# Kernel optimization log

Hardware: AMD Instinct MI355X
Metric: run time of the kernel (lower is better)

## Reference

```python
import jax, jax.numpy as jnp
import numpy as np

H = 64  # hidden_size
E = 100  # ebd_size
MAX_LEN = 100


def setup_inputs() -> dict:
    key = jax.random.key(0)
    ks = jax.random.split(key, 7)
    B, L = 4096, 100
    return {
        "x": jax.random.normal(ks[0], (B, L, E), jnp.float32),
        "W_in": jax.random.normal(ks[1], (E, 3 * H), jnp.float32) * 0.1,
        "b_in": jax.random.normal(ks[2], (3 * H,), jnp.float32) * 0.1,
        "W_h": jax.random.normal(ks[3], (H, 3 * H), jnp.float32) * 0.1,
        "b_h": jax.random.normal(ks[4], (3 * H,), jnp.float32) * 0.1,
        "W_fc": jax.random.normal(ks[5], (H, 2), jnp.float32) * 0.1,
        "b_fc": jax.random.normal(ks[6], (2,), jnp.float32) * 0.1,
    }


def _standardize(t):
    # torch: (t - t.mean(1, keepdim)) / t.std(1, keepdim)  (std is unbiased, ddof=1)
    m = jnp.mean(t, axis=1, keepdims=True)
    s = jnp.std(t, axis=1, keepdims=True, ddof=1)
    return (t - m) / s


def _gru_step(h, xt, W_in, b_in, W_h, b_h, norm):
    ti = xt @ W_in + b_in            # [B, 3H]
    th = h @ W_h + b_h               # [B, 3H]
    if norm:
        ti = _standardize(ti)
        th = _standardize(th)
    r_i, z_i, n_i = jnp.split(ti, 3, axis=1)
    r_h, z_h, n_h = jnp.split(th, 3, axis=1)
    r_t = jax.nn.sigmoid(r_i + r_h)
    z_t = jax.nn.sigmoid(z_i + z_h)
    n_t = jnp.tanh(n_i + r_t * n_h)
    return (1.0 - z_t) * n_t + z_t * h


def reference(x, W_in, b_in, W_h, b_h, W_fc, b_fc):
    B, L, _ = x.shape
    L_eff = min(L, MAX_LEN + 1)  # loop breaks when l > max_length
    xs = jnp.transpose(x[:, :L_eff, :], (1, 0, 2))  # [L, B, E]
    h0 = jnp.zeros((B, H), x.dtype)

    # loop 1: no norm
    h1, _ = jax.lax.scan(
        lambda h, xt: (_gru_step(h, xt, W_in, b_in, W_h, b_h, norm=False), None),
        h0, xs)
    # loop 2: vector norm; note original code does NOT reset hid_i
    h2, _ = jax.lax.scan(
        lambda h, xt: (_gru_step(h, xt, W_in, b_in, W_h, b_h, norm=True), None),
        h1, xs)
    return h2 @ W_fc + b_fc
```

## Files before the change

kernel.cpp:

```cpp
#include <hip/hip_runtime.h>

#define L_SEQ 100
#define E_DIM 100
#define G_DIM 192
#define B_TOT 4096

typedef __attribute__((ext_vector_type(8))) short bf16x8;
typedef __attribute__((ext_vector_type(4))) float f32x4;
typedef __attribute__((ext_vector_type(4))) float float4v;
typedef __attribute__((ext_vector_type(2))) float float2v;
typedef __attribute__((ext_vector_type(4))) unsigned uint4v;
typedef __attribute__((ext_vector_type(2))) unsigned uint2v;

#define MFMA16 __builtin_amdgcn_mfma_f32_16x16x32_bf16

static __device__ __forceinline__ unsigned short f2bf(float f) {
    union { float f; unsigned u; } v; v.f = f;
    unsigned r = v.u + 0x7FFFu + ((v.u >> 16) & 1u);
    return (unsigned short)(r >> 16);
}
static __device__ __forceinline__ unsigned cvtpk(float lo, float hi) {
    unsigned r;
    asm("v_cvt_pk_bf16_f32 %0, %1, %2" : "=v"(r) : "v"(lo), "v"(hi));
    return r;
}
static __device__ __forceinline__ bf16x8 as_bf16x8(uint4v u) {
    union { uint4v u; bf16x8 h; } v; v.u = u; return v.h;
}
static __device__ __forceinline__ float rcpf_(float x) { return __builtin_amdgcn_rcpf(x); }

#define BAR() do { \
    asm volatile("s_waitcnt lgkmcnt(0)" ::: "memory"); \
    __builtin_amdgcn_s_barrier(); \
    asm volatile("" ::: "memory"); \
} while (0)

struct XBuf { f32x4 v[6]; f32x4 tail; };

static __device__ __forceinline__ int tmod(int c) {
    int t = c;
    if (t >= L_SEQ) t -= L_SEQ;
    if (t >= L_SEQ) t -= L_SEQ;
    return t;
}

static __device__ __forceinline__ void x_pf(
    XBuf& b, const float* __restrict__ xlane, const float* __restrict__ xrow, int c, bool g0)
{
    const int t = tmod(c);
    const float* p = xlane + t * E_DIM;
    b.v[0] = *(const f32x4*)(p);
    b.v[1] = *(const f32x4*)(p + 4);
    b.v[2] = *(const f32x4*)(p + 32);
    b.v[3] = *(const f32x4*)(p + 36);
    b.v[4] = *(const f32x4*)(p + 64);
    b.v[5] = *(const f32x4*)(p + 68);
    const f32x4 z = {0.f, 0.f, 0.f, 0.f};
    b.tail = g0 ? *(const f32x4*)(xrow + t * E_DIM + 96) : z;
}

static __device__ __forceinline__ void produce(
    XBuf& xb, const float* __restrict__ xlane, const float* __restrict__ xrow,
    int c, bool g0, float* __restrict__ tird, float* __restrict__ sltiw,
    const bf16x8 (&awin)[3][4], const float (&binq)[12])
{
    bf16x8 bx0 = as_bf16x8((uint4v){cvtpk(xb.v[0][0], xb.v[0][1]), cvtpk(xb.v[0][2], xb.v[0][3]),
                                    cvtpk(xb.v[1][0], xb.v[1][1]), cvtpk(xb.v[1][2], xb.v[1][3])});
    bf16x8 bx1 = as_bf16x8((uint4v){cvtpk(xb.v[2][0], xb.v[2][1]), cvtpk(xb.v[2][2], xb.v[2][3]),
                                    cvtpk(xb.v[3][0], xb.v[3][1]), cvtpk(xb.v[3][2], xb.v[3][3])});
    bf16x8 bx2 = as_bf16x8((uint4v){cvtpk(xb.v[4][0], xb.v[4][1]), cvtpk(xb.v[4][2], xb.v[4][3]),
                                    cvtpk(xb.v[5][0], xb.v[5][1]), cvtpk(xb.v[5][2], xb.v[5][3])});
    bf16x8 bx3 = as_bf16x8((uint4v){cvtpk(xb.tail[0], xb.tail[1]), cvtpk(xb.tail[2], xb.tail[3]),
                                    0u, 0u});
    x_pf(xb, xlane, xrow, c + 2, g0);

    const f32x4 zero = {0.f, 0.f, 0.f, 0.f};
    f32x4 t0 = MFMA16(awin[0][0], bx0, zero, 0, 0, 0);
    f32x4 t1 = MFMA16(awin[1][0], bx0, zero, 0, 0, 0);
    f32x4 t2 = MFMA16(awin[2][0], bx0, zero, 0, 0, 0);
    t0 = MFMA16(awin[0][1], bx1, t0, 0, 0, 0);
    t1 = MFMA16(awin[1][1], bx1, t1, 0, 0, 0);
    t2 = MFMA16(awin[2][1], bx1, t2, 0, 0, 0);
    t0 = MFMA16(awin[0][2], bx2, t0, 0, 0, 0);
    t1 = MFMA16(awin[1][2], bx2, t1, 0, 0, 0);
    t2 = MFMA16(awin[2][2], bx2, t2, 0, 0, 0);
    t0 = MFMA16(awin[0][3], bx3, t0, 0, 0, 0);
    t1 = MFMA16(awin[1][3], bx3, t1, 0, 0, 0);
    t2 = MFMA16(awin[2][3], bx3, t2, 0, 0, 0);

    const int par = c & 1;
    float4v A0 = {t0[0] + binq[0], t0[1] + binq[1], t0[2] + binq[2],  t0[3] + binq[3]};
    float4v A1 = {t1[0] + binq[4], t1[1] + binq[5], t1[2] + binq[6],  t1[3] + binq[7]};
    float4v A2 = {t2[0] + binq[8], t2[1] + binq[9], t2[2] + binq[10], t2[3] + binq[11]};
    float* dst = tird + par * 3328;
    *(float4v*)(dst)     = A0;
    *(float4v*)(dst + 4) = A1;
    *(float4v*)(dst + 8) = A2;

    float s = ((A0[0] + A0[1]) + (A0[2] + A0[3])) + ((A1[0] + A1[1]) + (A1[2] + A1[3]))
            + ((A2[0] + A2[1]) + (A2[2] + A2[3]));
    float ss = 0.f;
    #pragma unroll
    for (int k2 = 0; k2 < 4; ++k2) ss = fmaf(A0[k2], A0[k2], ss);
    #pragma unroll
    for (int k2 = 0; k2 < 4; ++k2) ss = fmaf(A1[k2], A1[k2], ss);
    #pragma unroll
    for (int k2 = 0; k2 < 4; ++k2) ss = fmaf(A2[k2], A2[k2], ss);
    s  += __shfl_xor(s, 16);  s  += __shfl_xor(s, 32);
    ss += __shfl_xor(ss, 16); ss += __shfl_xor(ss, 32);
    if (g0) *(float2v*)(sltiw + par * 192) = (float2v){s, ss};
}

__global__ __launch_bounds__(512, 1) void gru_ws(
    const float* __restrict__ x,
    const float* __restrict__ Win, const float* __restrict__ bin,
    const float* __restrict__ Wh,  const float* __restrict__ bh,
    const float* __restrict__ Wfc, const float* __restrict__ bfc,
    float* __restrict__ out)
{
    __shared__ __align__(16) unsigned short hs[2][16][72];
    __shared__ __align__(16) float tir[2][4][16][52];
    __shared__ __align__(16) float slti[2][16][12];
    __shared__ __align__(16) float slth[2][16][12];

    const int tid = threadIdx.x;
    const int wv  = tid >> 6;
    const int w   = wv & 3;
    const bool tirole = (wv >= 4);
    const int l = tid & 63, c16 = l & 15, g = l >> 4;
    const bool g0 = (g == 0);
    const int row0 = blockIdx.x * 16;

    bf16x8 awin[3][4]; float binq[12];
    bf16x8 awh[3][2];  float bhq[12];
    const float* xrow = nullptr; const float* xlane = nullptr;

    if (tirole) {
        #pragma unroll
        for (int i = 0; i < 3; ++i)
          #pragma unroll
          for (int kt = 0; kt < 4; ++kt)
            #pragma unroll
            for (int j = 0; j < 8; ++j) {
                int k = 32 * kt + 8 * g + j;
                float v = (k < E_DIM) ? Win[k * G_DIM + 16 * (w + 4 * i) + c16] : 0.f;
                awin[i][kt][j] = (short)f2bf(v);
            }
        #pragma unroll
        for (int i = 0; i < 3; ++i)
          #pragma unroll
          for (int rr = 0; rr < 4; ++rr)
              binq[4 * i + rr] = bin[16 * (w + 4 * i) + 4 * g + rr];
        xrow  = x + (size_t)(row0 + c16) * (L_SEQ * E_DIM);
        xlane = xrow + 8 * g;
    } else {
        #pragma unroll
        for (int i = 0; i < 3; ++i)
          #pragma unroll
          for (int kt = 0; kt < 2; ++kt)
            #pragma unroll
            for (int j = 0; j < 8; ++j)
                awh[i][kt][j] = (short)f2bf(Wh[(32 * kt + 8 * g + j) * G_DIM + 16 * (w + 4 * i) + c16]);
        #pragma unroll
        for (int i = 0; i < 3; ++i)
          #pragma unroll
          for (int rr = 0; rr < 4; ++rr)
              bhq[4 * i + rr] = bh[16 * (w + 4 * i) + 4 * g + rr];
        bf16x8 z = {0, 0, 0, 0, 0, 0, 0, 0};
        *(bf16x8*)&hs[0][c16][8 * g]      = z;
        *(bf16x8*)&hs[0][c16][32 + 8 * g] = z;
    }

    float* tird        = &tir[0][w][c16][g * 12];
    float* sltiw       = &slti[0][c16][2 * w];
    float* slthw       = &slth[0][c16][2 * w];
    const float* sltir = &slti[0][c16][0];
    const float* slthr = &slth[0][c16][0];

    float hreg[4] = {0.f, 0.f, 0.f, 0.f};

    XBuf xA, xB;
    if (tirole) {
        x_pf(xA, xlane, xrow, 0, g0);
        x_pf(xB, xlane, xrow, 1, g0);
        produce(xA, xlane, xrow, 0, g0, tird, sltiw, awin, binq);
    }
    BAR();
    if (!tirole) __builtin_amdgcn_s_setprio(1);

    auto HGEMM = [&](int par, float4v& a0, float4v& a1, float4v& a2, float (&b)[12]) {
        const float* src = tird + par * 3328;
        a0 = *(const float4v*)(src);
        a1 = *(const float4v*)(src + 4);
        a2 = *(const float4v*)(src + 8);
        bf16x8 h0 = *(const bf16x8*)&hs[par][c16][8 * g];
        bf16x8 h1 = *(const bf16x8*)&hs[par][c16][32 + 8 * g];
        const f32x4 zero = {0.f, 0.f, 0.f, 0.f};
        f32x4 t0 = MFMA16(awh[0][0], h0, zero, 0, 0, 0);
        f32x4 t1 = MFMA16(awh[1][0], h0, zero, 0, 0, 0);
        f32x4 t2 = MFMA16(awh[2][0], h0, zero, 0, 0, 0);
        t0 = MFMA16(awh[0][1], h1, t0, 0, 0, 0);
        t1 = MFMA16(awh[1][1], h1, t1, 0, 0, 0);
        t2 = MFMA16(awh[2][1], h1, t2, 0, 0, 0);
        #pragma unroll
        for (int rr = 0; rr < 4; ++rr) {
            b[rr]     = t0[rr] + bhq[rr];
            b[4 + rr] = t1[rr] + bhq[4 + rr];
            b[8 + rr] = t2[rr] + bhq[8 + rr];
        }
    };
    auto HWRITE = [&](int par, float (&hn)[4]) {
        *(uint2v*)&hs[par ^ 1][c16][16 * w + 4 * g] = (uint2v){cvtpk(hn[0], hn[1]), cvtpk(hn[2], hn[3])};
    };

    #pragma unroll 1
    for (int s = 0; s < L_SEQ; s += 2) {
        #pragma unroll
        for (int sub = 0; sub < 2; ++sub) {
            const int st = s + sub;
            XBuf& X = sub ? xA : xB;
            if (tirole) {
                produce(X, xlane, xrow, st + 1, g0, tird, sltiw, awin, binq);
            } else {
                const int par = st & 1;
                float4v a0, a1, a2; float b[12];
                HGEMM(par, a0, a1, a2, b);
                float hn[4];
                #pragma unroll
                for (int rr = 0; rr < 4; ++rr) {
                    float er = rcpf_(1.f + __expf(-(a0[rr] + b[rr])));
                    float zt = rcpf_(1.f + __expf(-(a1[rr] + b[4 + rr])));
                    float u  = fmaf(er, b[8 + rr], a2[rr]);
                    float tn = fmaf(2.f, rcpf_(1.f + __expf(-2.f * u)), -1.f);
                    hn[rr] = fmaf(zt, hreg[rr] - tn, tn);
                    hreg[rr] = hn[rr];
                }
                HWRITE(par, hn);
            }
            BAR();
        }
    }

    #pragma unroll 1
    for (int s = L_SEQ; s < 2 * L_SEQ; s += 2) {
        #pragma unroll
        for (int sub = 0; sub < 2; ++sub) {
            const int st = s + sub;
            XBuf& X = sub ? xA : xB;
            const int par = st & 1;
            float4v a0, a1, a2; float b[12];
            if (tirole) {
                produce(X, xlane, xrow, st + 1, g0, tird, sltiw, awin, binq);
            } else {
                HGEMM(par, a0, a1, a2, b);
                float sb = 0.f, ssb = 0.f;
                #pragma unroll
                for (int k2 = 0; k2 < 12; ++k2) { sb += b[k2]; ssb = fmaf(b[k2], b[k2], ssb); }
                sb  += __shfl_xor(sb, 16);  sb  += __shfl_xor(sb, 32);
                ssb += __shfl_xor(ssb, 16); ssb += __shfl_xor(ssb, 32);
                if (g0) *(float2v*)(slthw + par * 192) = (float2v){sb, ssb};
            }
            BAR();
            if (!tirole) {
                const float* sp = slthr + par * 192;
                float4v q0 = *(const float4v*)(sp);
                float4v q1 = *(const float4v*)(sp + 4);
                const float* ip = sltir + par * 192;
                float4v r0 = *(const float4v*)(ip);
                float4v r1 = *(const float4v*)(ip + 4);
                float Sth  = (q0[0] + q0[2]) + (q1[0] + q1[2]);
                float SSth = (q0[1] + q0[3]) + (q1[1] + q1[3]);
                float Sti  = (r0[0] + r0[2]) + (r1[0] + r1[2]);
                float SSti = (r0[1] + r0[3]) + (r1[1] + r1[3]);
                float mth = Sth * (1.f / G_DIM);
                float rth = __builtin_amdgcn_rsqf(
                    fmaxf((SSth - (float)G_DIM * mth * mth) * (1.f / (G_DIM - 1)), 1e-24f));
                float mti = Sti * (1.f / G_DIM);
                float rti = __builtin_amdgcn_rsqf(
                    fmaxf((SSti - (float)G_DIM * mti * mti) * (1.f / (G_DIM - 1)), 1e-24f));
                float mrti = mti * rti, mrth = mth * rth;
                float Cn = mrti + mrth;
                float hn[4];
                #pragma unroll
                for (int rr = 0; rr < 4; ++rr) {
                    float mr = fmaf(a0[rr], -rti, fmaf(b[rr],     -rth, Cn));
                    float er = rcpf_(1.f + __expf(mr));
                    float mz = fmaf(a1[rr], -rti, fmaf(b[4 + rr], -rth, Cn));
                    float zt = rcpf_(1.f + __expf(mz));
                    float ni = fmaf(a2[rr],     rti, -mrti);
                    float nh = fmaf(b[8 + rr],  rth, -mrth);
                    float u  = fmaf(er, nh, ni);
                    float tn = fmaf(2.f, rcpf_(1.f + __expf(-2.f * u)), -1.f);
                    hn[rr] = fmaf(zt, hreg[rr] - tn, tn);
                    hreg[rr] = hn[rr];
                }
                HWRITE(par, hn);
            }
            BAR();
        }
    }

    if (!tirole) {
        float po0 = 0.f, po1 = 0.f;
        #pragma unroll
        for (int rr = 0; rr < 4; ++rr) {
            int c = 16 * w + 4 * g + rr;
            po0 = fmaf(hreg[rr], Wfc[2 * c],     po0);
            po1 = fmaf(hreg[rr], Wfc[2 * c + 1], po1);
        }
        po0 += __shfl_xor(po0, 16); po0 += __shfl_xor(po0, 32);
        po1 += __shfl_xor(po1, 16); po1 += __shfl_xor(po1, 32);
        if (g0) *(float2v*)(slthw) = (float2v){po0, po1};
    }
    BAR();
    if (tid < 16) {
        const float* sp = &slth[0][tid][0];
        float4v q0 = *(const float4v*)(sp);
        float4v q1 = *(const float4v*)(sp + 4);
        out[(row0 + tid) * 2 + 0] = (q0[0] + q0[2]) + (q1[0] + q1[2]) + bfc[0];
        out[(row0 + tid) * 2 + 1] = (q0[1] + q0[3]) + (q1[1] + q1[3]) + bfc[1];
    }
}

extern "C" void kernel_launch(void* const* d_in, const int* in_sizes, int n_in,
                              void* d_out, int out_size, void* d_ws, size_t ws_size,
                              hipStream_t stream) {
    const float* x   = (const float*)d_in[0];
    const float* Win = (const float*)d_in[1];
    const float* bin = (const float*)d_in[2];
    const float* Wh  = (const float*)d_in[3];
    const float* bh  = (const float*)d_in[4];
    const float* Wfc = (const float*)d_in[5];
    const float* bfc = (const float*)d_in[6];
    float* out = (float*)d_out;
    gru_ws<<<dim3(B_TOT / 16), dim3(512), 0, stream>>>(
        x, Win, bin, Wh, bh, Wfc, bfc, out);
}
```

Measured before the change: 201.0 us.

## Prefetch input-gate projections one step ahead and fold log2e into weights

Producer warps now run two steps ahead instead of one. The recurrent warps load the next step's input-gate values and input-norm statistics right after writing h, instead of at the start of the next step. The input-side mean and rstd are precomputed inside that prefetch. All weights and biases are pre-scaled by log2(e) so the activations can use exp2 directly, which removes a multiply per exponent. This changes the slot/parity scheme and the barrier structure, and it risks extra register pressure plus bf16 rounding differences from the scaled weights.

New measurement: 238.3 us. +18.5%, slower.

```diff
diff --git a/kernel.cpp b/kernel.cpp
--- a/kernel.cpp
+++ b/kernel.cpp
@@ -4,6 +4,7 @@
 #define E_DIM 100
 #define G_DIM 192
 #define B_TOT 4096
+#define L2E   1.4426950408889634f
 
 typedef __attribute__((ext_vector_type(8))) short bf16x8;
 typedef __attribute__((ext_vector_type(4))) float f32x4;
@@ -36,9 +37,11 @@
 } while (0)
 
 struct XBuf { f32x4 v[6]; f32x4 tail; };
+struct TiRegs { float4v a0, a1, a2; float rtiF, cF; };
 
 static __device__ __forceinline__ int tmod(int c) {
     int t = c;
+    if (t >= L_SEQ) t -= L_SEQ;
     if (t >= L_SEQ) t -= L_SEQ;
     if (t >= L_SEQ) t -= L_SEQ;
     return t;
@@ -111,6 +114,25 @@
     if (g0) *(float2v*)(sltiw + par * 192) = (float2v){s, ss};
 }
 
+static __device__ __forceinline__ void lr_load(
+    TiRegs& R, int slot, const float* __restrict__ tird, const float* __restrict__ sltir)
+{
+    const float* src = tird + slot * 3328;
+    R.a0 = *(const float4v*)(src);
+    R.a1 = *(const float4v*)(src + 4);
+    R.a2 = *(const float4v*)(src + 8);
+    const float* sp = sltir + slot * 192;
+    float4v q0 = *(const float4v*)(sp);
+    float4v q1 = *(const float4v*)(sp + 4);
+    float S  = (q0[0] + q0[2]) + (q1[0] + q1[2]);
+    float SS = (q0[1] + q0[3]) + (q1[1] + q1[3]);
+    float m  = S * (1.f / G_DIM);
+    float var = (SS - (float)G_DIM * m * m) * (1.f / (G_DIM - 1));
+    float r = __builtin_amdgcn_rsqf(fmaxf(var, 1e-24f)) * L2E;
+    R.rtiF = r;
+    R.cF   = m * r;
+}
+
 __global__ __launch_bounds__(512, 1) void gru_ws(
     const float* __restrict__ x,
     const float* __restrict__ Win, const float* __restrict__ bin,
@@ -132,7 +154,7 @@
     const int row0 = blockIdx.x * 16;
 
     bf16x8 awin[3][4]; float binq[12];
-    bf16x8 awh[3][2];  float bhq[12];
+    bf16x8 awh[3][2];  float bhqL[12];
     const float* xrow = nullptr; const float* xlane = nullptr;
 
     if (tirole) {
@@ -143,14 +165,14 @@
             #pragma unroll
             for (int j = 0; j < 8; ++j) {
                 int k = 32 * kt + 8 * g + j;
-                float v = (k < E_DIM) ? Win[k * G_DIM + 16 * (w + 4 * i) + c16] : 0.f;
+                float v = (k < E_DIM) ? Win[k * G_DIM + 16 * (w + 4 * i) + c16] * L2E : 0.f;
                 awin[i][kt][j] = (short)f2bf(v);
             }
         #pragma unroll
         for (int i = 0; i < 3; ++i)
           #pragma unroll
           for (int rr = 0; rr < 4; ++rr)
-              binq[4 * i + rr] = bin[16 * (w + 4 * i) + 4 * g + rr];
+              binq[4 * i + rr] = bin[16 * (w + 4 * i) + 4 * g + rr] * L2E;
         xrow  = x + (size_t)(row0 + c16) * (L_SEQ * E_DIM);
         xlane = xrow + 8 * g;
     } else {
@@ -160,12 +182,12 @@
           for (int kt = 0; kt < 2; ++kt)
             #pragma unroll
             for (int j = 0; j < 8; ++j)
-                awh[i][kt][j] = (short)f2bf(Wh[(32 * kt + 8 * g + j) * G_DIM + 16 * (w + 4 * i) + c16]);
+                awh[i][kt][j] = (short)f2bf(Wh[(32 * kt + 8 * g + j) * G_DIM + 16 * (w + 4 * i) + c16] * L2E);
         #pragma unroll
         for (int i = 0; i < 3; ++i)
           #pragma unroll
           for (int rr = 0; rr < 4; ++rr)
-              bhq[4 * i + rr] = bh[16 * (w + 4 * i) + 4 * g + rr];
+              bhqL[4 * i + rr] = bh[16 * (w + 4 * i) + 4 * g + rr] * L2E;
         bf16x8 z = {0, 0, 0, 0, 0, 0, 0, 0};
         *(bf16x8*)&hs[0][c16][8 * g]      = z;
         *(bf16x8*)&hs[0][c16][32 + 8 * g] = z;
@@ -184,15 +206,17 @@
         x_pf(xA, xlane, xrow, 0, g0);
         x_pf(xB, xlane, xrow, 1, g0);
         produce(xA, xlane, xrow, 0, g0, tird, sltiw, awin, binq);
+        produce(xB, xlane, xrow, 1, g0, tird, sltiw, awin, binq);
     }
     BAR();
-    if (!tirole) __builtin_amdgcn_s_setprio(1);
-
-    auto HGEMM = [&](int par, float4v& a0, float4v& a1, float4v& a2, float (&b)[12]) {
-        const float* src = tird + par * 3328;
-        a0 = *(const float4v*)(src);
-        a1 = *(const float4v*)(src + 4);
-        a2 = *(const float4v*)(src + 8);
+
+    TiRegs RA, RB;
+    if (!tirole) {
+        lr_load(RA, 0, tird, sltir);
+        __builtin_amdgcn_s_setprio(1);
+    }
+
+    auto HGEMM = [&](int par, float (&b)[12]) {
         bf16x8 h0 = *(const bf16x8*)&hs[par][c16][8 * g];
         bf16x8 h1 = *(const bf16x8*)&hs[par][c16][32 + 8 * g];
         const f32x4 zero = {0.f, 0.f, 0.f, 0.f};
@@ -204,100 +228,91 @@
         t2 = MFMA16(awh[2][1], h1, t2, 0, 0, 0);
         #pragma unroll
         for (int rr = 0; rr < 4; ++rr) {
-            b[rr]     = t0[rr] + bhq[rr];
-            b[4 + rr] = t1[rr] + bhq[4 + rr];
-            b[8 + rr] = t2[rr] + bhq[8 + rr];
+            b[rr]     = t0[rr] + bhqL[rr];
+            b[4 + rr] = t1[rr] + bhqL[4 + rr];
+            b[8 + rr] = t2[rr] + bhqL[8 + rr];
         }
     };
     auto HWRITE = [&](int par, float (&hn)[4]) {
         *(uint2v*)&hs[par ^ 1][c16][16 * w + 4 * g] = (uint2v){cvtpk(hn[0], hn[1]), cvtpk(hn[2], hn[3])};
     };
 
+    auto H1 = [&](TiRegs& CUR, TiRegs& NXT, int st) {
+        const int par = st & 1;
+        float b[12];
+        HGEMM(par, b);
+        float hn[4];
+        #pragma unroll
+        for (int rr = 0; rr < 4; ++rr) {
+            float er = rcpf_(1.f + __builtin_exp2f(-(CUR.a0[rr] + b[rr])));
+            float zt = rcpf_(1.f + __builtin_exp2f(-(CUR.a1[rr] + b[4 + rr])));
+            float uL = fmaf(er, b[8 + rr], CUR.a2[rr]);
+            float tn = fmaf(2.f, rcpf_(1.f + __builtin_exp2f(-(uL + uL))), -1.f);
+            hn[rr] = fmaf(zt, hreg[rr] - tn, tn);
+            hreg[rr] = hn[rr];
+        }
+        HWRITE(par, hn);
+        lr_load(NXT, (st + 1) & 1, tird, sltir);
+    };
+
     #pragma unroll 1
     for (int s = 0; s < L_SEQ; s += 2) {
-        #pragma unroll
-        for (int sub = 0; sub < 2; ++sub) {
-            const int st = s + sub;
-            XBuf& X = sub ? xA : xB;
-            if (tirole) {
-                produce(X, xlane, xrow, st + 1, g0, tird, sltiw, awin, binq);
-            } else {
-                const int par = st & 1;
-                float4v a0, a1, a2; float b[12];
-                HGEMM(par, a0, a1, a2, b);
-                float hn[4];
-                #pragma unroll
-                for (int rr = 0; rr < 4; ++rr) {
-                    float er = rcpf_(1.f + __expf(-(a0[rr] + b[rr])));
-                    float zt = rcpf_(1.f + __expf(-(a1[rr] + b[4 + rr])));
-                    float u  = fmaf(er, b[8 + rr], a2[rr]);
-                    float tn = fmaf(2.f, rcpf_(1.f + __expf(-2.f * u)), -1.f);
-                    hn[rr] = fmaf(zt, hreg[rr] - tn, tn);
-                    hreg[rr] = hn[rr];
-                }
-                HWRITE(par, hn);
-            }
-            BAR();
+        if (tirole) produce(xA, xlane, xrow, s + 2, g0, tird, sltiw, awin, binq);
+        else        H1(RA, RB, s);
+        BAR();
+        if (tirole) produce(xB, xlane, xrow, s + 3, g0, tird, sltiw, awin, binq);
+        else        H1(RB, RA, s + 1);
+        BAR();
+    }
+
+    auto H2 = [&](TiRegs& CUR, TiRegs& NXT, int st) {
+        const int par = st & 1;
+        float b[12];
+        HGEMM(par, b);
+        float sb = 0.f, ssb = 0.f;
+        #pragma unroll
+        for (int k2 = 0; k2 < 12; ++k2) { sb += b[k2]; ssb = fmaf(b[k2], b[k2], ssb); }
+        sb  += __shfl_xor(sb, 16);  sb  += __shfl_xor(sb, 32);
+        ssb += __shfl_xor(ssb, 16); ssb += __shfl_xor(ssb, 32);
+        if (g0) *(float2v*)(slthw + par * 192) = (float2v){sb, ssb};
+        BAR();
+        const float* sp = slthr + par * 192;
+        float4v q0 = *(const float4v*)(sp);
+        float4v q1 = *(const float4v*)(sp + 4);
+        float S  = (q0[0] + q0[2]) + (q1[0] + q1[2]);
+        float SS = (q0[1] + q0[3]) + (q1[1] + q1[3]);
+        float m  = S * (1.f / G_DIM);
+        float var = (SS - (float)G_DIM * m * m) * (1.f / (G_DIM - 1));
+        float rthF = __builtin_amdgcn_rsqf(fmaxf(var, 1e-24f)) * L2E;
+        float chF  = m * rthF;
+        float hn[4];
+        #pragma unroll
+        for (int rr = 0; rr < 4; ++rr) {
+            float ntr = fmaf(CUR.a0[rr], CUR.rtiF, -CUR.cF);
+            float ntz = fmaf(CUR.a1[rr], CUR.rtiF, -CUR.cF);
+            float ntn = fmaf(CUR.a2[rr], CUR.rtiF, -CUR.cF);
+            float nhr = fmaf(b[rr],     rthF, -chF);
+            float nhz = fmaf(b[4 + rr], rthF, -chF);
+            float nhn = fmaf(b[8 + rr], rthF, -chF);
+            float er = rcpf_(1.f + __builtin_exp2f(-(ntr + nhr)));
+            float zt = rcpf_(1.f + __builtin_exp2f(-(ntz + nhz)));
+            float uL = fmaf(er, nhn, ntn);
+            float tn = fmaf(2.f, rcpf_(1.f + __builtin_exp2f(-(uL + uL))), -1.f);
+            hn[rr] = fmaf(zt, hreg[rr] - tn, tn);
+            hreg[rr] = hn[rr];
         }
-    }
+        HWRITE(par, hn);
+        lr_load(NXT, (st + 1) & 1, tird, sltir);
+    };
 
     #pragma unroll 1
     for (int s = L_SEQ; s < 2 * L_SEQ; s += 2) {
-        #pragma unroll
-        for (int sub = 0; sub < 2; ++sub) {
-            const int st = s + sub;
-            XBuf& X = sub ? xA : xB;
-            const int par = st & 1;
-            float4v a0, a1, a2; float b[12];
-            if (tirole) {
-                produce(X, xlane, xrow, st + 1, g0, tird, sltiw, awin, binq);
-            } else {
-                HGEMM(par, a0, a1, a2, b);
-                float sb = 0.f, ssb = 0.f;
-                #pragma unroll
-                for (int k2 = 0; k2 < 12; ++k2) { sb += b[k2]; ssb = fmaf(b[k2], b[k2], ssb); }
-                sb  += __shfl_xor(sb, 16);  sb  += __shfl_xor(sb, 32);
-                ssb += __shfl_xor(ssb, 16); ssb += __shfl_xor(ssb, 32);
-                if (g0) *(float2v*)(slthw + par * 192) = (float2v){sb, ssb};
-            }
-            BAR();
-            if (!tirole) {
-                const float* sp = slthr + par * 192;
-                float4v q0 = *(const float4v*)(sp);
-                float4v q1 = *(const float4v*)(sp + 4);
-                const float* ip = sltir + par * 192;
-                float4v r0 = *(const float4v*)(ip);
-                float4v r1 = *(const float4v*)(ip + 4);
-                float Sth  = (q0[0] + q0[2]) + (q1[0] + q1[2]);
-                float SSth = (q0[1] + q0[3]) + (q1[1] + q1[3]);
-                float Sti  = (r0[0] + r0[2]) + (r1[0] + r1[2]);
-                float SSti = (r0[1] + r0[3]) + (r1[1] + r1[3]);
-                float mth = Sth * (1.f / G_DIM);
-                float rth = __builtin_amdgcn_rsqf(
-                    fmaxf((SSth - (float)G_DIM * mth * mth) * (1.f / (G_DIM - 1)), 1e-24f));
-                float mti = Sti * (1.f / G_DIM);
-                float rti = __builtin_amdgcn_rsqf(
-                    fmaxf((SSti - (float)G_DIM * mti * mti) * (1.f / (G_DIM - 1)), 1e-24f));
-                float mrti = mti * rti, mrth = mth * rth;
-                float Cn = mrti + mrth;
-                float hn[4];
-                #pragma unroll
-                for (int rr = 0; rr < 4; ++rr) {
-                    float mr = fmaf(a0[rr], -rti, fmaf(b[rr],     -rth, Cn));
-                    float er = rcpf_(1.f + __expf(mr));
-                    float mz = fmaf(a1[rr], -rti, fmaf(b[4 + rr], -rth, Cn));
-                    float zt = rcpf_(1.f + __expf(mz));
-                    float ni = fmaf(a2[rr],     rti, -mrti);
-                    float nh = fmaf(b[8 + rr],  rth, -mrth);
-                    float u  = fmaf(er, nh, ni);
-                    float tn = fmaf(2.f, rcpf_(1.f + __expf(-2.f * u)), -1.f);
-                    hn[rr] = fmaf(zt, hreg[rr] - tn, tn);
-                    hreg[rr] = hn[rr];
-                }
-                HWRITE(par, hn);
-            }
-            BAR();
-        }
+        if (tirole) { produce(xA, xlane, xrow, s + 2, g0, tird, sltiw, awin, binq); BAR(); }
+        else        H2(RA, RB, s);
+        BAR();
+        if (tirole) { produce(xB, xlane, xrow, s + 3, g0, tird, sltiw, awin, binq); BAR(); }
+        else        H2(RB, RA, s + 1);
+        BAR();
     }
 
     if (!tirole) {
```

## Compute hidden-gate norm stats algebraically via Gram matrix, removing a barrier

Applied to the files above, without the earlier changes.

Precomputes the Gram matrix Wh·Whᵀ, the row sums of Wh and Wh·bh in shared memory, so each wave computes the sum and sum of squares of h@Wh+bh locally from h with extra MFMAs instead of doing a cross-wave reduction through LDS. This removes one of the two barriers per step in the normalized loop. The cost is extra MFMA and register work per step, a Gram-matrix prologue, and different rounding from bf16 h, with possible cancellation in the variance formula.

Measured after the change: 432.7 us. 2.15x slower.

```diff
diff --git a/kernel.cpp b/kernel.cpp
--- a/kernel.cpp
+++ b/kernel.cpp
@@ -11,6 +11,7 @@
 typedef __attribute__((ext_vector_type(2))) float float2v;
 typedef __attribute__((ext_vector_type(4))) unsigned uint4v;
 typedef __attribute__((ext_vector_type(2))) unsigned uint2v;
+typedef __attribute__((ext_vector_type(4))) unsigned short ushort4v;
 
 #define MFMA16 __builtin_amdgcn_mfma_f32_16x16x32_bf16
 
@@ -18,6 +19,10 @@
     union { float f; unsigned u; } v; v.f = f;
     unsigned r = v.u + 0x7FFFu + ((v.u >> 16) & 1u);
     return (unsigned short)(r >> 16);
+}
+static __device__ __forceinline__ float bf2f(unsigned short u) {
+    union { unsigned u; float f; } v; v.u = ((unsigned)u) << 16;
+    return v.f;
 }
 static __device__ __forceinline__ unsigned cvtpk(float lo, float hi) {
     unsigned r;
@@ -39,6 +44,7 @@
 
 static __device__ __forceinline__ int tmod(int c) {
     int t = c;
+    if (t >= L_SEQ) t -= L_SEQ;
     if (t >= L_SEQ) t -= L_SEQ;
     if (t >= L_SEQ) t -= L_SEQ;
     return t;
@@ -122,6 +128,10 @@
     __shared__ __align__(16) float tir[2][4][16][52];
     __shared__ __align__(16) float slti[2][16][12];
     __shared__ __align__(16) float slth[2][16][12];
+    __shared__ __align__(16) float Ms[64][65];
+    __shared__ __align__(16) float wsumS[64];
+    __shared__ __align__(16) float vS[64];
+    __shared__ float sbhS[2];
 
     const int tid = threadIdx.x;
     const int wv  = tid >> 6;
@@ -131,8 +141,52 @@
     const bool g0 = (g == 0);
     const int row0 = blockIdx.x * 16;
 
+    {
+        #pragma unroll 1
+        for (int e8 = 0; e8 < 8; ++e8) {
+            int e = (tid << 3) + e8;
+            int kk = e >> 6, dd = e & 63;
+            const float* wk = Wh + kk * G_DIM;
+            const float* wd = Wh + dd * G_DIM;
+            float acc = 0.f;
+            #pragma unroll 4
+            for (int c = 0; c < G_DIM; c += 4) {
+                float4v a = *(const float4v*)(wk + c);
+                float4v b = *(const float4v*)(wd + c);
+                #pragma unroll
+                for (int q = 0; q < 4; ++q) acc = fmaf(a[q], b[q], acc);
+            }
+            Ms[kk][dd] = acc;
+        }
+        if (tid < 64) {
+            const float* wr = Wh + tid * G_DIM;
+            float s = 0.f, sv = 0.f;
+            #pragma unroll 4
+            for (int c = 0; c < G_DIM; ++c) {
+                s += wr[c];
+                sv = fmaf(wr[c], bh[c], sv);
+            }
+            wsumS[tid] = s;
+            vS[tid] = sv;
+        }
+        if (tid == 64) {
+            float sb = 0.f, sq = 0.f;
+            #pragma unroll 4
+            for (int c = 0; c < G_DIM; ++c) {
+                sb += bh[c];
+                sq = fmaf(bh[c], bh[c], sq);
+            }
+            sbhS[0] = sb;
+            sbhS[1] = sq;
+        }
+    }
+    BAR();
+
     bf16x8 awin[3][4]; float binq[12];
     bf16x8 awh[3][2];  float bhq[12];
+    bf16x8 awm[4][2];  float wsumq[16];
+    f32x4 vC0, vC1, vC2, vC3;
+    float sum_bh = 0.f, ssq_bh = 0.f;
     const float* xrow = nullptr; const float* xlane = nullptr;
 
     if (tirole) {
@@ -166,6 +220,27 @@
           #pragma unroll
           for (int rr = 0; rr < 4; ++rr)
               bhq[4 * i + rr] = bh[16 * (w + 4 * i) + 4 * g + rr];
+        #pragma unroll
+        for (int nt = 0; nt < 4; ++nt)
+          #pragma unroll
+          for (int kt = 0; kt < 2; ++kt)
+            #pragma unroll
+            for (int j = 0; j < 8; ++j)
+                awm[nt][kt][j] = (short)f2bf(Ms[32 * kt + 8 * g + j][16 * nt + c16]);
+        #pragma unroll
+        for (int q = 0; q < 8; ++q) {
+            wsumq[q]     = wsumS[8 * g + q];
+            wsumq[8 + q] = wsumS[32 + 8 * g + q];
+        }
+        #pragma unroll
+        for (int rr = 0; rr < 4; ++rr) {
+            vC0[rr] = 2.f * vS[ 0 + 4 * g + rr];
+            vC1[rr] = 2.f * vS[16 + 4 * g + rr];
+            vC2[rr] = 2.f * vS[32 + 4 * g + rr];
+            vC3[rr] = 2.f * vS[48 + 4 * g + rr];
+        }
+        sum_bh = sbhS[0];
+        ssq_bh = sbhS[1];
         bf16x8 z = {0, 0, 0, 0, 0, 0, 0, 0};
         *(bf16x8*)&hs[0][c16][8 * g]      = z;
         *(bf16x8*)&hs[0][c16][32 + 8 * g] = z;
@@ -175,7 +250,6 @@
     float* sltiw       = &slti[0][c16][2 * w];
     float* slthw       = &slth[0][c16][2 * w];
     const float* sltir = &slti[0][c16][0];
-    const float* slthr = &slth[0][c16][0];
 
     float hreg[4] = {0.f, 0.f, 0.f, 0.f};
 
@@ -188,11 +262,7 @@
     BAR();
     if (!tirole) __builtin_amdgcn_s_setprio(1);
 
-    auto HGEMM = [&](int par, float4v& a0, float4v& a1, float4v& a2, float (&b)[12]) {
-        const float* src = tird + par * 3328;
-        a0 = *(const float4v*)(src);
-        a1 = *(const float4v*)(src + 4);
-        a2 = *(const float4v*)(src + 8);
+    auto HGEMM = [&](int par, float (&b)[12]) {
         bf16x8 h0 = *(const bf16x8*)&hs[par][c16][8 * g];
         bf16x8 h1 = *(const bf16x8*)&hs[par][c16][32 + 8 * g];
         const f32x4 zero = {0.f, 0.f, 0.f, 0.f};
@@ -213,91 +283,130 @@
         *(uint2v*)&hs[par ^ 1][c16][16 * w + 4 * g] = (uint2v){cvtpk(hn[0], hn[1]), cvtpk(hn[2], hn[3])};
     };
 
+    auto H1 = [&](int st) {
+        const int par = st & 1;
+        const float* src = tird + par * 3328;
+        float4v a0 = *(const float4v*)(src);
+        float4v a1 = *(const float4v*)(src + 4);
+        float4v a2 = *(const float4v*)(src + 8);
+        float b[12];
+        HGEMM(par, b);
+        float hn[4];
+        #pragma unroll
+        for (int rr = 0; rr < 4; ++rr) {
+            float er = rcpf_(1.f + __expf(-(a0[rr] + b[rr])));
+            float zt = rcpf_(1.f + __expf(-(a1[rr] + b[4 + rr])));
+            float u  = fmaf(er, b[8 + rr], a2[rr]);
+            float tn = fmaf(2.f, rcpf_(1.f + __expf(-2.f * u)), -1.f);
+            hn[rr] = fmaf(zt, hreg[rr] - tn, tn);
+            hreg[rr] = hn[rr];
+        }
+        HWRITE(par, hn);
+    };
+
     #pragma unroll 1
     for (int s = 0; s < L_SEQ; s += 2) {
-        #pragma unroll
-        for (int sub = 0; sub < 2; ++sub) {
-            const int st = s + sub;
-            XBuf& X = sub ? xA : xB;
-            if (tirole) {
-                produce(X, xlane, xrow, st + 1, g0, tird, sltiw, awin, binq);
-            } else {
-                const int par = st & 1;
-                float4v a0, a1, a2; float b[12];
-                HGEMM(par, a0, a1, a2, b);
-                float hn[4];
-                #pragma unroll
-                for (int rr = 0; rr < 4; ++rr) {
-                    float er = rcpf_(1.f + __expf(-(a0[rr] + b[rr])));
-                    float zt = rcpf_(1.f + __expf(-(a1[rr] + b[4 + rr])));
-                    float u  = fmaf(er, b[8 + rr], a2[rr]);
-                    float tn = fmaf(2.f, rcpf_(1.f + __expf(-2.f * u)), -1.f);
-                    hn[rr] = fmaf(zt, hreg[rr] - tn, tn);
-                    hreg[rr] = hn[rr];
-                }
-                HWRITE(par, hn);
-            }
-            BAR();
-        }
-    }
+        if (tirole) produce(xB, xlane, xrow, s + 1, g0, tird, sltiw, awin, binq);
+        else        H1(s);
+        BAR();
+        if (tirole) produce(xA, xlane, xrow, s + 2, g0, tird, sltiw, awin, binq);
+        else        H1(s + 1);
+        BAR();
+    }
+
+    auto H2 = [&](int st) {
+        const int par = st & 1;
+        const float* src = tird + par * 3328;
+        float4v a0 = *(const float4v*)(src);
+        float4v a1 = *(const float4v*)(src + 4);
+        float4v a2 = *(const float4v*)(src + 8);
+        const float* ip = sltir + par * 192;
+        float4v r0 = *(const float4v*)(ip);
+        float4v r1 = *(const float4v*)(ip + 4);
+        float Sti  = (r0[0] + r0[2]) + (r1[0] + r1[2]);
+        float SSti = (r0[1] + r0[3]) + (r1[1] + r1[3]);
+        float mti  = Sti * (1.f / G_DIM);
+        float vti  = (SSti - (float)G_DIM * mti * mti) * (1.f / (G_DIM - 1));
+        float rti  = __builtin_amdgcn_rsqf(fmaxf(vti, 1e-24f));
+
+        bf16x8 h0 = *(const bf16x8*)&hs[par][c16][8 * g];
+        bf16x8 h1 = *(const bf16x8*)&hs[par][c16][32 + 8 * g];
+        ushort4v hq0 = *(const ushort4v*)&hs[par][c16][4 * g];
+        ushort4v hq1 = *(const ushort4v*)&hs[par][c16][16 + 4 * g];
+        ushort4v hq2 = *(const ushort4v*)&hs[par][c16][32 + 4 * g];
+        ushort4v hq3 = *(const ushort4v*)&hs[par][c16][48 + 4 * g];
+        const f32x4 zero = {0.f, 0.f, 0.f, 0.f};
+        f32x4 t0 = MFMA16(awh[0][0], h0, zero, 0, 0, 0);
+        f32x4 t1 = MFMA16(awh[1][0], h0, zero, 0, 0, 0);
+        f32x4 t2 = MFMA16(awh[2][0], h0, zero, 0, 0, 0);
+        t0 = MFMA16(awh[0][1], h1, t0, 0, 0, 0);
+        t1 = MFMA16(awh[1][1], h1, t1, 0, 0, 0);
+        t2 = MFMA16(awh[2][1], h1, t2, 0, 0, 0);
+        f32x4 u0 = MFMA16(awm[0][0], h0, vC0, 0, 0, 0);
+        f32x4 u1 = MFMA16(awm[1][0], h0, vC1, 0, 0, 0);
+        f32x4 u2 = MFMA16(awm[2][0], h0, vC2, 0, 0, 0);
+        f32x4 u3 = MFMA16(awm[3][0], h0, vC3, 0, 0, 0);
+        u0 = MFMA16(awm[0][1], h1, u0, 0, 0, 0);
+        u1 = MFMA16(awm[1][1], h1, u1, 0, 0, 0);
+        u2 = MFMA16(awm[2][1], h1, u2, 0, 0, 0);
+        u3 = MFMA16(awm[3][1], h1, u3, 0, 0, 0);
+
+        float b[12];
+        #pragma unroll
+        for (int rr = 0; rr < 4; ++rr) {
+            b[rr]     = t0[rr] + bhq[rr];
+            b[4 + rr] = t1[rr] + bhq[4 + rr];
+            b[8 + rr] = t2[rr] + bhq[8 + rr];
+        }
+        float sS = 0.f;
+        #pragma unroll
+        for (int q = 0; q < 8; ++q) {
+            sS = fmaf(bf2f((unsigned short)h0[q]), wsumq[q],     sS);
+            sS = fmaf(bf2f((unsigned short)h1[q]), wsumq[8 + q], sS);
+        }
+        float sSS = 0.f;
+        #pragma unroll
+        for (int rr = 0; rr < 4; ++rr) {
+            sSS = fmaf(bf2f(hq0[rr]), u0[rr], sSS);
+            sSS = fmaf(bf2f(hq1[rr]), u1[rr], sSS);
+            sSS = fmaf(bf2f(hq2[rr]), u2[rr], sSS);
+            sSS = fmaf(bf2f(hq3[rr]), u3[rr], sSS);
+        }
+        sS  += __shfl_xor(sS, 16);  sS  += __shfl_xor(sS, 32);
+        sSS += __shfl_xor(sSS, 16); sSS += __shfl_xor(sSS, 32);
+        float S   = sS + sum_bh;
+        float SSf = sSS + ssq_bh;
+        float mth = S * (1.f / G_DIM);
+        float var = (SSf - (float)G_DIM * mth * mth) * (1.f / (G_DIM - 1));
+        float rth = __builtin_amdgcn_rsqf(fmaxf(var, 1e-24f));
+
+        float mrti = mti * rti, mrth = mth * rth;
+        float Cn = mrti + mrth;
+        float hn[4];
+        #pragma unroll
+        for (int rr = 0; rr < 4; ++rr) {
+            float mr = fmaf(a0[rr], -rti, fmaf(b[rr],     -rth, Cn));
+            float er = rcpf_(1.f + __expf(mr));
+            float mz = fmaf(a1[rr], -rti, fmaf(b[4 + rr], -rth, Cn));
+            float zt = rcpf_(1.f + __expf(mz));
+            float ni = fmaf(a2[rr],     rti, -mrti);
+            float nh = fmaf(b[8 + rr],  rth, -mrth);
+            float u  = fmaf(er, nh, ni);
+            float tn = fmaf(2.f, rcpf_(1.f + __expf(-2.f * u)), -1.f);
+            hn[rr] = fmaf(zt, hreg[rr] - tn, tn);
+            hreg[rr] = hn[rr];
+        }
+        HWRITE(par, hn);
+    };
 
     #pragma unroll 1
     for (int s = L_SEQ; s < 2 * L_SEQ; s += 2) {
-        #pragma unroll
-        for (int sub = 0; sub < 2; ++sub) {
-            const int st = s + sub;
-            XBuf& X = sub ? xA : xB;
-            const int par = st & 1;
-            float4v a0, a1, a2; float b[12];
-            if (tirole) {
-                produce(X, xlane, xrow, st + 1, g0, tird, sltiw, awin, binq);
-            } else {
-                HGEMM(par, a0, a1, a2, b);
-                float sb = 0.f, ssb = 0.f;
-                #pragma unroll
-                for (int k2 = 0; k2 < 12; ++k2) { sb += b[k2]; ssb = fmaf(b[k2], b[k2], ssb); }
-                sb  += __shfl_xor(sb, 16);  sb  += __shfl_xor(sb, 32);
-                ssb += __shfl_xor(ssb, 16); ssb += __shfl_xor(ssb, 32);
-                if (g0) *(float2v*)(slthw + par * 192) = (float2v){sb, ssb};
-            }
-            BAR();
-            if (!tirole) {
-                const float* sp = slthr + par * 192;
-                float4v q0 = *(const float4v*)(sp);
-                float4v q1 = *(const float4v*)(sp + 4);
-                const float* ip = sltir + par * 192;
-                float4v r0 = *(const float4v*)(ip);
-                float4v r1 = *(const float4v*)(ip + 4);
-                float Sth  = (q0[0] + q0[2]) + (q1[0] + q1[2]);
-                float SSth = (q0[1] + q0[3]) + (q1[1] + q1[3]);
-                float Sti  = (r0[0] + r0[2]) + (r1[0] + r1[2]);
-                float SSti = (r0[1] + r0[3]) + (r1[1] + r1[3]);
-                float mth = Sth * (1.f / G_DIM);
-                float rth = __builtin_amdgcn_rsqf(
-                    fmaxf((SSth - (float)G_DIM * mth * mth) * (1.f / (G_DIM - 1)), 1e-24f));
-                float mti = Sti * (1.f / G_DIM);
-                float rti = __builtin_amdgcn_rsqf(
-                    fmaxf((SSti - (float)G_DIM * mti * mti) * (1.f / (G_DIM - 1)), 1e-24f));
-                float mrti = mti * rti, mrth = mth * rth;
-                float Cn = mrti + mrth;
-                float hn[4];
-                #pragma unroll
-                for (int rr = 0; rr < 4; ++rr) {
-                    float mr = fmaf(a0[rr], -rti, fmaf(b[rr],     -rth, Cn));
-                    float er = rcpf_(1.f + __expf(mr));
-                    float mz = fmaf(a1[rr], -rti, fmaf(b[4 + rr], -rth, Cn));
-                    float zt = rcpf_(1.f + __expf(mz));
-                    float ni = fmaf(a2[rr],     rti, -mrti);
-                    float nh = fmaf(b[8 + rr],  rth, -mrth);
-                    float u  = fmaf(er, nh, ni);
-                    float tn = fmaf(2.f, rcpf_(1.f + __expf(-2.f * u)), -1.f);
-                    hn[rr] = fmaf(zt, hreg[rr] - tn, tn);
-                    hreg[rr] = hn[rr];
-                }
-                HWRITE(par, hn);
-            }
-            BAR();
-        }
+        if (tirole) produce(xB, xlane, xrow, s + 1, g0, tird, sltiw, awin, binq);
+        else        H2(s);
+        BAR();
+        if (tirole) produce(xA, xlane, xrow, s + 2, g0, tird, sltiw, awin, binq);
+        else        H2(s + 1);
+        BAR();
     }
 
     if (!tirole) {
```
